# Performance work log

Measured on AMD Instinct MI355X. Metric: run time of the kernel, lower is better.

Reference implementation:

```python
import jax, jax.numpy as jnp
import numpy as np

N = 1_000_000
H = 64   # hidden_dim
E = 4    # edge_dim
S = 3    # state_dim


def _linear_params(key, fan_in, fan_out):
    kw, kb = jax.random.split(key)
    bound = 1.0 / np.sqrt(fan_in)
    W = jax.random.uniform(kw, (fan_in, fan_out), jnp.float32, -bound, bound)
    b = jax.random.uniform(kb, (fan_out,), jnp.float32, -bound, bound)
    return W, b


def setup_inputs() -> dict:
    key = jax.random.key(0)
    k_pc, k1, k2, k3, kmu, klam = jax.random.split(key, 6)
    W1, b1 = _linear_params(k1, 2, H)
    W2, b2 = _linear_params(k2, H, H)
    W3, b3 = _linear_params(k3, H, H)
    Wmu, bmu = _linear_params(kmu, H, E)
    Wlam, blam = _linear_params(klam, H, S)
    point_cloud = jax.random.normal(k_pc, (N, 2), jnp.float32)
    return {
        "point_cloud": point_cloud,
        "W1": W1, "b1": b1,
        "W2": W2, "b2": b2,
        "W3": W3, "b3": b3,
        "Wmu": Wmu, "bmu": bmu,
        "Wlam": Wlam, "blam": blam,
    }


def reference(point_cloud, W1, b1, W2, b2, W3, b3, Wmu, bmu, Wlam, blam):
    # Fixed constraint matrix G (edge_dim x state_dim)
    G = jnp.array([[1.0, 0.0, 0.0],
                   [-1.0, 0.0, 0.0],
                   [0.0, 1.0, 0.0],
                   [0.0, -1.0, 0.0]], dtype=jnp.float32)

    # MLP encoder: (N,2) -> (N,H)
    h = jax.nn.relu(point_cloud @ W1 + b1)
    h = jax.nn.relu(h @ W2 + b2)
    h = jax.nn.relu(h @ W3 + b3)

    mu = (h @ Wmu + bmu).T     # (E, N)
    lam = (h @ Wlam + blam).T  # (S, N)

    # Hard projection for mu: relu, then per-column clip of ||G^T mu||_2 to <= 1.
    # Vectorized replacement of the original per-column Python loop.
    mu = jax.nn.relu(mu)
    gtm = G.T @ mu                               # (S, N)
    norm = jnp.linalg.norm(gtm, axis=0)          # (N,)
    scale = jnp.where(norm > 1.0, 1.0 / (norm + 1e-8), 1.0)
    mu = mu * scale[None, :]

    # Hard projection for lam: always normalize each column to unit norm.
    lam = lam / (jnp.linalg.norm(lam, axis=0, keepdims=True) + 1e-8)
    return mu, lam
```

## Files before the change

kernel.cpp:

```cpp
#include <hip/hip_runtime.h>

typedef _Float16 h2 __attribute__((ext_vector_type(2)));
typedef _Float16 h8 __attribute__((ext_vector_type(8)));
typedef float    f4 __attribute__((ext_vector_type(4)));

#define PI(t,r) (8*((r)>>2) + ((r)&3) + 4*((t)&1) + 32*((t)>>1))

#define FSTRIDE 29

union Frag { h8 v; h2 q[4]; f4 f; };

__device__ __forceinline__ h2 relu2(h2 a) {
    const h2 z = {};
    return __builtin_elementwise_max(a, z);
}

__device__ __forceinline__ h2 pkrtz(float a, float b) {
    return __builtin_bit_cast(h2, __builtin_amdgcn_cvt_pkrtz(a, b));
}

__device__ __forceinline__ void packB(const f4 (&a)[4], Frag (&B)[2]) {
    #pragma unroll
    for (int c = 0; c < 2; ++c) {
        #pragma unroll
        for (int hh = 0; hh < 2; ++hh) {
            const int t = 2*c + hh;
            B[c].q[2*hh + 0] = relu2(pkrtz(a[t][0], a[t][1]));
            B[c].q[2*hh + 1] = relu2(pkrtz(a[t][2], a[t][3]));
        }
    }
}

__global__ __launch_bounds__(256, 2)
void pihp_mfma(const float* __restrict__ pc,
               const float* __restrict__ W1, const float* __restrict__ b1,
               const float* __restrict__ W2, const float* __restrict__ b2,
               const float* __restrict__ W3, const float* __restrict__ b3,
               const float* __restrict__ Wmu, const float* __restrict__ bmu,
               const float* __restrict__ Wlam, const float* __restrict__ blam,
               float* __restrict__ out, int N)
{
    __shared__ f4 wblob[64 * FSTRIDE];

    const int tid  = threadIdx.x;
    const int lane = tid & 63;
    const int g    = lane >> 4;
    const int m    = lane & 15;
    const int sec  = tid >> 6;

    f4* myw = &wblob[lane * FSTRIDE];
    if (sec == 0) {
        #pragma unroll
        for (int t = 0; t < 2; ++t)
            #pragma unroll
            for (int c = 0; c < 2; ++c) {
                Frag fr;
                #pragma unroll
                for (int ii = 0; ii < 8; ++ii)
                    fr.v[ii] = (_Float16)W2[(32*c + 8*g + ii)*64 + PI(t, m)];
                myw[2*t + c] = fr.f;
            }
        #pragma unroll
        for (int c = 0; c < 2; ++c) {
            Frag fr;
            #pragma unroll
            for (int ii = 0; ii < 8; ++ii) {
                const int k = 32*c + 8*g + ii;
                float v = 0.0f;
                if (m < 4)      v = Wmu[k*4 + m];
                else if (m < 7) v = Wlam[k*3 + (m - 4)];
                fr.v[ii] = (_Float16)v;
            }
            myw[16 + c] = fr.f;
        }
    } else if (sec == 1) {
        #pragma unroll
        for (int t = 2; t < 4; ++t)
            #pragma unroll
            for (int c = 0; c < 2; ++c) {
                Frag fr;
                #pragma unroll
                for (int ii = 0; ii < 8; ++ii)
                    fr.v[ii] = (_Float16)W2[(32*c + 8*g + ii)*64 + PI(t, m)];
                myw[2*t + c] = fr.f;
            }
        #pragma unroll
        for (int t = 0; t < 4; ++t) {
            f4 bb;
            #pragma unroll
            for (int i = 0; i < 4; ++i) bb[i] = b2[PI(t, 4*g + i)];
            myw[18 + t] = bb;
        }
    } else if (sec == 2) {
        #pragma unroll
        for (int t = 0; t < 2; ++t)
            #pragma unroll
            for (int c = 0; c < 2; ++c) {
                Frag fr;
                #pragma unroll
                for (int ii = 0; ii < 8; ++ii)
                    fr.v[ii] = (_Float16)W3[(32*c + 8*g + ii)*64 + PI(t, m)];
                myw[8 + 2*t + c] = fr.f;
            }
        #pragma unroll
        for (int t = 0; t < 4; ++t) {
            f4 bb;
            #pragma unroll
            for (int i = 0; i < 4; ++i) bb[i] = b3[PI(t, 4*g + i)];
            myw[22 + t] = bb;
        }
    } else {
        #pragma unroll
        for (int t = 2; t < 4; ++t)
            #pragma unroll
            for (int c = 0; c < 2; ++c) {
                Frag fr;
                #pragma unroll
                for (int ii = 0; ii < 8; ++ii)
                    fr.v[ii] = (_Float16)W3[(32*c + 8*g + ii)*64 + PI(t, m)];
                myw[8 + 2*t + c] = fr.f;
            }
        f4 bb;
        #pragma unroll
        for (int i = 0; i < 4; ++i) {
            const int rr = 4*g + i;
            bb[i] = (rr < 4) ? bmu[rr] : (rr < 7 ? blam[rr - 4] : 0.0f);
        }
        myw[26] = bb;
    }

    h2 w1x[2][4], w1y[2][4], w1b[2][4];
    #pragma unroll
    for (int c = 0; c < 2; ++c)
        #pragma unroll
        for (int p = 0; p < 4; ++p) {
            const int k = 32*c + 8*g + 2*p;
            w1x[c][p][0] = (_Float16)W1[k];      w1x[c][p][1] = (_Float16)W1[k+1];
            w1y[c][p][0] = (_Float16)W1[64+k];   w1y[c][p][1] = (_Float16)W1[64+k+1];
            w1b[c][p][0] = (_Float16)b1[k];      w1b[c][p][1] = (_Float16)b1[k+1];
        }

    __syncthreads();

    h8 A2f[4][2], A3f[4][2], Ahf[2];
    f4 bC2[4], bC3[4], bCh;
    #pragma unroll
    for (int t = 0; t < 4; ++t)
        #pragma unroll
        for (int c = 0; c < 2; ++c) {
            A2f[t][c] = __builtin_bit_cast(h8, myw[2*t + c]);
            A3f[t][c] = __builtin_bit_cast(h8, myw[8 + 2*t + c]);
        }
    #pragma unroll
    for (int c = 0; c < 2; ++c) Ahf[c] = __builtin_bit_cast(h8, myw[16 + c]);
    #pragma unroll
    for (int t = 0; t < 4; ++t) { bC2[t] = myw[18 + t]; bC3[t] = myw[22 + t]; }
    bCh = myw[26];

    #pragma unroll
    for (int t = 0; t < 4; ++t)
        #pragma unroll
        for (int c = 0; c < 2; ++c) {
            asm volatile("" : "+v"(A2f[t][c]));
            asm volatile("" : "+v"(A3f[t][c]));
        }
    #pragma unroll
    for (int c = 0; c < 2; ++c) asm volatile("" : "+v"(Ahf[c]));
    #pragma unroll
    for (int t = 0; t < 4; ++t) {
        asm volatile("" : "+v"(bC2[t]));
        asm volatile("" : "+v"(bC3[t]));
    }
    asm volatile("" : "+v"(bCh));

    const int wid = blockIdx.x * (blockDim.x >> 6) + sec;
    const int nw  = gridDim.x * (blockDim.x >> 6);
    const int nslab = (N + 15) >> 4;
    int per = (nslab + nw - 1) / nw;
    per = (per + 1) & ~1;
    const int s0 = wid * per;
    if (s0 >= nslab) return;
    const int s1 = (s0 + per < nslab) ? (s0 + per) : nslab;

    float* const pl0 = out;
    float* const pl1 = out + (size_t)N;
    float* const pl2 = out + (size_t)2*N;
    float* const pl3 = out + (size_t)3*N;
    float* const pl4 = out + (size_t)4*N;
    float* const pl5 = out + (size_t)5*N;
    float* const pl6 = out + (size_t)6*N;

    const float2* __restrict__ pcv = reinterpret_cast<const float2*>(pc);
    const int Nm1 = N - 1;
    auto clampload = [&](int ss) -> float2 {
        int pt = ss*16 + m;
        pt = pt < Nm1 ? pt : Nm1;
        return pcv[pt];
    };

    float2 Pc0 = clampload(s0);
    float2 Pc1 = clampload(s0 + 1);
    const bool isMu = (g == 0);

    #pragma unroll 1
    for (int ss = s0; ss < s1; ss += 2) {
        float2 Pn0 = clampload(ss + 2);
        float2 Pn1 = clampload(ss + 3);

        Frag B0[2], B1[2];
        {
            const h2 x0 = pkrtz(Pc0.x, Pc0.x), y0 = pkrtz(Pc0.y, Pc0.y);
            const h2 x1 = pkrtz(Pc1.x, Pc1.x), y1 = pkrtz(Pc1.y, Pc1.y);
            #pragma unroll
            for (int c = 0; c < 2; ++c)
                #pragma unroll
                for (int p = 0; p < 4; ++p) {
                    B0[c].q[p] = relu2(x0 * w1x[c][p] + y0 * w1y[c][p] + w1b[c][p]);
                    B1[c].q[p] = relu2(x1 * w1x[c][p] + y1 * w1y[c][p] + w1b[c][p]);
                }
        }

        f4 a0[4], a1[4];

        #pragma unroll
        for (int t = 0; t < 4; ++t) {
            a0[t] = __builtin_amdgcn_mfma_f32_16x16x32_f16(A2f[t][0], B0[0].v, bC2[t], 0, 0, 0);
            a1[t] = __builtin_amdgcn_mfma_f32_16x16x32_f16(A2f[t][0], B1[0].v, bC2[t], 0, 0, 0);
        }
        #pragma unroll
        for (int t = 0; t < 4; ++t) {
            a0[t] = __builtin_amdgcn_mfma_f32_16x16x32_f16(A2f[t][1], B0[1].v, a0[t], 0, 0, 0);
            a1[t] = __builtin_amdgcn_mfma_f32_16x16x32_f16(A2f[t][1], B1[1].v, a1[t], 0, 0, 0);
        }
        packB(a0, B0);
        packB(a1, B1);

        #pragma unroll
        for (int t = 0; t < 4; ++t) {
            a0[t] = __builtin_amdgcn_mfma_f32_16x16x32_f16(A3f[t][0], B0[0].v, bC3[t], 0, 0, 0);
            a1[t] = __builtin_amdgcn_mfma_f32_16x16x32_f16(A3f[t][0], B1[0].v, bC3[t], 0, 0, 0);
        }
        #pragma unroll
        for (int t = 0; t < 4; ++t) {
            a0[t] = __builtin_amdgcn_mfma_f32_16x16x32_f16(A3f[t][1], B0[1].v, a0[t], 0, 0, 0);
            a1[t] = __builtin_amdgcn_mfma_f32_16x16x32_f16(A3f[t][1], B1[1].v, a1[t], 0, 0, 0);
        }
        packB(a0, B0);
        packB(a1, B1);

        f4 h0, h1;
        h0 = __builtin_amdgcn_mfma_f32_16x16x32_f16(Ahf[0], B0[0].v, bCh, 0, 0, 0);
        h1 = __builtin_amdgcn_mfma_f32_16x16x32_f16(Ahf[0], B1[0].v, bCh, 0, 0, 0);
        h0 = __builtin_amdgcn_mfma_f32_16x16x32_f16(Ahf[1], B0[1].v, h0, 0, 0, 0);
        h1 = __builtin_amdgcn_mfma_f32_16x16x32_f16(Ahf[1], B1[1].v, h1, 0, 0, 0);

        #pragma unroll
        for (int u = 0; u < 2; ++u) {
            const f4 hv = (u == 0) ? h0 : h1;
            const int pt = (ss + u)*16 + m;
            const float r0 = isMu ? fmaxf(hv[0], 0.0f) : hv[0];
            const float r1 = isMu ? fmaxf(hv[1], 0.0f) : hv[1];
            const float r2 = isMu ? fmaxf(hv[2], 0.0f) : hv[2];
            const float r3 = isMu ? fmaxf(hv[3], 0.0f) : hv[3];
            const float t0 = isMu ? (r0 - r1) : r0;
            const float t1 = isMu ? (r2 - r3) : r1;
            const float t2 = isMu ? 0.0f      : r2;
            const float ssum = t0*t0 + t1*t1 + t2*t2;
            const float r  = rsqrtf(ssum + 1e-16f);
            const float sc = isMu ? fminf(r, 1.0f) : r;
            if (g == 0) {
                pl0[pt] = r0 * sc;
                pl1[pt] = r1 * sc;
                pl2[pt] = r2 * sc;
                pl3[pt] = r3 * sc;
            } else if (g == 1) {
                pl4[pt] = r0 * sc;
                pl5[pt] = r1 * sc;
                pl6[pt] = r2 * sc;
            }
        }

        Pc0 = Pn0;
        Pc1 = Pn1;
    }
}

extern "C" void kernel_launch(void* const* d_in, const int* in_sizes, int n_in,
                              void* d_out, int out_size, void* d_ws, size_t ws_size,
                              hipStream_t stream) {
    const float* pc   = (const float*)d_in[0];
    const float* W1   = (const float*)d_in[1];
    const float* b1   = (const float*)d_in[2];
    const float* W2   = (const float*)d_in[3];
    const float* b2   = (const float*)d_in[4];
    const float* W3   = (const float*)d_in[5];
    const float* b3   = (const float*)d_in[6];
    const float* Wmu  = (const float*)d_in[7];
    const float* bmu  = (const float*)d_in[8];
    const float* Wlam = (const float*)d_in[9];
    const float* blam = (const float*)d_in[10];
    float* out = (float*)d_out;

    const int N = in_sizes[0] / 2;
    pihp_mfma<<<512, 256, 0, stream>>>(pc, W1, b1, W2, b2, W3, b3,
                                       Wmu, bmu, Wlam, blam, out, N);
}
```

Baseline: 33.24 us.

## Software-pipeline MLP layers across slab pairs and reload biases from LDS

Restructures the main loop so layer 2 of the next slab pair runs interleaved with layer 3 of the current pair. This gives the MFMA pipe independent chains to hide dependency latency between layers. Bias accumulators are no longer pinned in registers; each iteration reads them from the shared weight buffer, which frees VGPRs to hold the extra pipelined state. The prologue computes layer 2 ahead of the loop and the point prefetch moves two slabs further ahead. Risks include higher register pressure, extra LDS reads, and extra tail work on clamped points.

Result: no change. 33.55 us (+0.9%).

```diff
diff --git a/kernel.cpp b/kernel.cpp
--- a/kernel.cpp
+++ b/kernel.cpp
@@ -143,7 +143,6 @@
     __syncthreads();
 
     h8 A2f[4][2], A3f[4][2], Ahf[2];
-    f4 bC2[4], bC3[4], bCh;
     #pragma unroll
     for (int t = 0; t < 4; ++t)
         #pragma unroll
@@ -154,10 +153,6 @@
     #pragma unroll
     for (int c = 0; c < 2; ++c) Ahf[c] = __builtin_bit_cast(h8, myw[16 + c]);
     #pragma unroll
-    for (int t = 0; t < 4; ++t) { bC2[t] = myw[18 + t]; bC3[t] = myw[22 + t]; }
-    bCh = myw[26];
-
-    #pragma unroll
     for (int t = 0; t < 4; ++t)
         #pragma unroll
         for (int c = 0; c < 2; ++c) {
@@ -166,12 +161,6 @@
         }
     #pragma unroll
     for (int c = 0; c < 2; ++c) asm volatile("" : "+v"(Ahf[c]));
-    #pragma unroll
-    for (int t = 0; t < 4; ++t) {
-        asm volatile("" : "+v"(bC2[t]));
-        asm volatile("" : "+v"(bC3[t]));
-    }
-    asm volatile("" : "+v"(bCh));
 
     const int wid = blockIdx.x * (blockDim.x >> 6) + sec;
     const int nw  = gridDim.x * (blockDim.x >> 6);
@@ -197,62 +186,86 @@
         pt = pt < Nm1 ? pt : Nm1;
         return pcv[pt];
     };
-
-    float2 Pc0 = clampload(s0);
-    float2 Pc1 = clampload(s0 + 1);
     const bool isMu = (g == 0);
+
+    auto stageL1 = [&](float2 P0, float2 P1, Frag (&Bx0)[2], Frag (&Bx1)[2]) {
+        const h2 x0 = pkrtz(P0.x, P0.x), y0 = pkrtz(P0.y, P0.y);
+        const h2 x1 = pkrtz(P1.x, P1.x), y1 = pkrtz(P1.y, P1.y);
+        #pragma unroll
+        for (int c = 0; c < 2; ++c)
+            #pragma unroll
+            for (int p = 0; p < 4; ++p) {
+                Bx0[c].q[p] = relu2(x0 * w1x[c][p] + y0 * w1y[c][p] + w1b[c][p]);
+                Bx1[c].q[p] = relu2(x1 * w1x[c][p] + y1 * w1y[c][p] + w1b[c][p]);
+            }
+    };
+
+    Frag Bm0[2], Bm1[2];
+    {
+        float2 P0 = clampload(s0), P1 = clampload(s0 + 1);
+        Frag Bi0[2], Bi1[2];
+        stageL1(P0, P1, Bi0, Bi1);
+        f4 a0[4], a1[4];
+        #pragma unroll
+        for (int t = 0; t < 4; ++t) {
+            const f4 bc = myw[18 + t];
+            a0[t] = __builtin_amdgcn_mfma_f32_16x16x32_f16(A2f[t][0], Bi0[0].v, bc, 0, 0, 0);
+            a1[t] = __builtin_amdgcn_mfma_f32_16x16x32_f16(A2f[t][0], Bi1[0].v, bc, 0, 0, 0);
+        }
+        #pragma unroll
+        for (int t = 0; t < 4; ++t) {
+            a0[t] = __builtin_amdgcn_mfma_f32_16x16x32_f16(A2f[t][1], Bi0[1].v, a0[t], 0, 0, 0);
+            a1[t] = __builtin_amdgcn_mfma_f32_16x16x32_f16(A2f[t][1], Bi1[1].v, a1[t], 0, 0, 0);
+        }
+        packB(a0, Bm0);
+        packB(a1, Bm1);
+    }
+    float2 Pc0 = clampload(s0 + 2);
+    float2 Pc1 = clampload(s0 + 3);
 
     #pragma unroll 1
     for (int ss = s0; ss < s1; ss += 2) {
-        float2 Pn0 = clampload(ss + 2);
-        float2 Pn1 = clampload(ss + 3);
-
-        Frag B0[2], B1[2];
+        asm volatile("" ::: "memory");
+
+        float2 Pn0 = clampload(ss + 4);
+        float2 Pn1 = clampload(ss + 5);
+
+        Frag Bi0[2], Bi1[2];
+        stageL1(Pc0, Pc1, Bi0, Bi1);
+
+        f4 aL3_0[4], aL3_1[4], aL2_0[4], aL2_1[4];
+        #pragma unroll
+        for (int t = 0; t < 4; ++t) {
+            const f4 b3c = myw[22 + t];
+            const f4 b2c = myw[18 + t];
+            aL3_0[t] = __builtin_amdgcn_mfma_f32_16x16x32_f16(A3f[t][0], Bm0[0].v, b3c, 0, 0, 0);
+            aL2_0[t] = __builtin_amdgcn_mfma_f32_16x16x32_f16(A2f[t][0], Bi0[0].v, b2c, 0, 0, 0);
+            aL3_1[t] = __builtin_amdgcn_mfma_f32_16x16x32_f16(A3f[t][0], Bm1[0].v, b3c, 0, 0, 0);
+            aL2_1[t] = __builtin_amdgcn_mfma_f32_16x16x32_f16(A2f[t][0], Bi1[0].v, b2c, 0, 0, 0);
+        }
+        #pragma unroll
+        for (int t = 0; t < 4; ++t) {
+            aL3_0[t] = __builtin_amdgcn_mfma_f32_16x16x32_f16(A3f[t][1], Bm0[1].v, aL3_0[t], 0, 0, 0);
+            aL2_0[t] = __builtin_amdgcn_mfma_f32_16x16x32_f16(A2f[t][1], Bi0[1].v, aL2_0[t], 0, 0, 0);
+            aL3_1[t] = __builtin_amdgcn_mfma_f32_16x16x32_f16(A3f[t][1], Bm1[1].v, aL3_1[t], 0, 0, 0);
+            aL2_1[t] = __builtin_amdgcn_mfma_f32_16x16x32_f16(A2f[t][1], Bi1[1].v, aL2_1[t], 0, 0, 0);
+        }
+
+        Frag Bo0[2], Bo1[2];
+        packB(aL3_0, Bo0);
+        packB(aL3_1, Bo1);
+
+        f4 h0, h1;
         {
-            const h2 x0 = pkrtz(Pc0.x, Pc0.x), y0 = pkrtz(Pc0.y, Pc0.y);
-            const h2 x1 = pkrtz(Pc1.x, Pc1.x), y1 = pkrtz(Pc1.y, Pc1.y);
-            #pragma unroll
-            for (int c = 0; c < 2; ++c)
-                #pragma unroll
-                for (int p = 0; p < 4; ++p) {
-                    B0[c].q[p] = relu2(x0 * w1x[c][p] + y0 * w1y[c][p] + w1b[c][p]);
-                    B1[c].q[p] = relu2(x1 * w1x[c][p] + y1 * w1y[c][p] + w1b[c][p]);
-                }
-        }
-
-        f4 a0[4], a1[4];
-
-        #pragma unroll
-        for (int t = 0; t < 4; ++t) {
-            a0[t] = __builtin_amdgcn_mfma_f32_16x16x32_f16(A2f[t][0], B0[0].v, bC2[t], 0, 0, 0);
-            a1[t] = __builtin_amdgcn_mfma_f32_16x16x32_f16(A2f[t][0], B1[0].v, bC2[t], 0, 0, 0);
-        }
-        #pragma unroll
-        for (int t = 0; t < 4; ++t) {
-            a0[t] = __builtin_amdgcn_mfma_f32_16x16x32_f16(A2f[t][1], B0[1].v, a0[t], 0, 0, 0);
-            a1[t] = __builtin_amdgcn_mfma_f32_16x16x32_f16(A2f[t][1], B1[1].v, a1[t], 0, 0, 0);
-        }
-        packB(a0, B0);
-        packB(a1, B1);
-
-        #pragma unroll
-        for (int t = 0; t < 4; ++t) {
-            a0[t] = __builtin_amdgcn_mfma_f32_16x16x32_f16(A3f[t][0], B0[0].v, bC3[t], 0, 0, 0);
-            a1[t] = __builtin_amdgcn_mfma_f32_16x16x32_f16(A3f[t][0], B1[0].v, bC3[t], 0, 0, 0);
-        }
-        #pragma unroll
-        for (int t = 0; t < 4; ++t) {
-            a0[t] = __builtin_amdgcn_mfma_f32_16x16x32_f16(A3f[t][1], B0[1].v, a0[t], 0, 0, 0);
-            a1[t] = __builtin_amdgcn_mfma_f32_16x16x32_f16(A3f[t][1], B1[1].v, a1[t], 0, 0, 0);
-        }
-        packB(a0, B0);
-        packB(a1, B1);
-
-        f4 h0, h1;
-        h0 = __builtin_amdgcn_mfma_f32_16x16x32_f16(Ahf[0], B0[0].v, bCh, 0, 0, 0);
-        h1 = __builtin_amdgcn_mfma_f32_16x16x32_f16(Ahf[0], B1[0].v, bCh, 0, 0, 0);
-        h0 = __builtin_amdgcn_mfma_f32_16x16x32_f16(Ahf[1], B0[1].v, h0, 0, 0, 0);
-        h1 = __builtin_amdgcn_mfma_f32_16x16x32_f16(Ahf[1], B1[1].v, h1, 0, 0, 0);
+            const f4 bch = myw[26];
+            h0 = __builtin_amdgcn_mfma_f32_16x16x32_f16(Ahf[0], Bo0[0].v, bch, 0, 0, 0);
+            h1 = __builtin_amdgcn_mfma_f32_16x16x32_f16(Ahf[0], Bo1[0].v, bch, 0, 0, 0);
+            h0 = __builtin_amdgcn_mfma_f32_16x16x32_f16(Ahf[1], Bo0[1].v, h0, 0, 0, 0);
+            h1 = __builtin_amdgcn_mfma_f32_16x16x32_f16(Ahf[1], Bo1[1].v, h1, 0, 0, 0);
+        }
+
+        packB(aL2_0, Bm0);
+        packB(aL2_1, Bm1);
 
         #pragma unroll
         for (int u = 0; u < 2; ++u) {
```
